# Kernel tuning notes

Hardware: AMD Instinct MI355X
Metric: run time of the kernel (lower is better)

Reference implementation:

```python
import jax, jax.numpy as jnp
import numpy as np

EPS = 1e-6
N_HEADS = 16
D_NOPE = 128   # qk_nope_head_dim == head_dim
D_ROPE = 64    # qk_rope_head_dim == head_dim // 2


def rmsnorm(x, g):
    # matches torch RMSNorm: normalize in fp32 then scale
    xf = x.astype(jnp.float32)
    n = xf * jax.lax.rsqrt(jnp.mean(xf * xf, axis=-1, keepdims=True) + EPS)
    return n.astype(x.dtype) * g


def rope(x):
    # x: [..., S, D]; rotary-embedding-torch convention: interleaved pairs, theta=10000
    S, D = x.shape[-2], x.shape[-1]
    freqs = 1.0 / (10000.0 ** (jnp.arange(0, D, 2, dtype=jnp.float32) / D))  # [D/2]
    ang = jnp.arange(S, dtype=jnp.float32)[:, None] * freqs                   # [S, D/2]
    ang = jnp.repeat(ang, 2, axis=-1)                                         # [S, D]
    cos, sin = jnp.cos(ang), jnp.sin(ang)
    x2 = x.reshape(*x.shape[:-1], D // 2, 2)
    xr = jnp.stack([-x2[..., 1], x2[..., 0]], axis=-1).reshape(x.shape)
    return x * cos + xr * sin


def setup_inputs() -> dict:
    key = jax.random.key(0)
    ks = jax.random.split(key, 9)
    def w(k, shape):
        return jax.random.normal(k, shape, dtype=jnp.float32) * (shape[0] ** -0.5)
    return {
        "x": jax.random.normal(ks[0], (2, 2048, 2048), dtype=jnp.float32),
        "w_dq": w(ks[1], (2048, 512)),
        "g_q": jnp.ones((512,), dtype=jnp.float32),
        "w_uq": w(ks[2], (512, 3072)),
        "w_dkv": w(ks[3], (2048, 512)),
        "g_kv": jnp.ones((512,), dtype=jnp.float32),
        "w_ukrope": w(ks[4], (2048, 64)),
        "w_uv": w(ks[5], (512, 2048)),
        "w_uknope": w(ks[6], (512, 2048)),
        "w_o": w(ks[7], (2048, 2048)),
    }


def reference(x, w_dq, g_q, w_uq, w_dkv, g_kv, w_ukrope, w_uv, w_uknope, w_o):
    B, S, _ = x.shape
    H, Dn, Dr = N_HEADS, D_NOPE, D_ROPE

    # low-rank KV path
    kv = rmsnorm(x @ w_dkv, g_kv)                                    # [B,S,512]
    k_nope = (kv @ w_uknope).reshape(B, S, H, Dn).transpose(0, 2, 1, 3)  # [B,H,S,Dn]
    v = (kv @ w_uv).reshape(B, S, H, Dn).transpose(0, 2, 1, 3)           # [B,H,S,Dn]
    k_rope = rope(x @ w_ukrope)                                      # [B,S,Dr] shared across heads

    # low-rank Q path
    q = rmsnorm(x @ w_dq, g_q) @ w_uq                                # [B,S,H*(Dn+Dr)]
    q = q.reshape(B, S, H, Dn + Dr).transpose(0, 2, 1, 3)            # [B,H,S,Dn+Dr]
    q_nope, q_rope = q[..., :Dn], rope(q[..., Dn:])

    # causal SDPA with head-shared rope keys folded into scores
    scale = 1.0 / jnp.sqrt(jnp.float32(Dn + Dr))
    scores = jnp.einsum("bhqd,bhkd->bhqk", q_nope, k_nope)
    scores = scores + jnp.einsum("bhqd,bkd->bhqk", q_rope, k_rope)
    scores = scores * scale
    causal = jnp.tril(jnp.ones((S, S), dtype=bool))
    scores = jnp.where(causal, scores, -jnp.inf)
    attn = jax.nn.softmax(scores, axis=-1)
    out = jnp.einsum("bhqk,bhkd->bhqd", attn, v)                     # [B,H,S,Dn]
    out = out.transpose(0, 2, 1, 3).reshape(B, S, H * Dn)
    return out @ w_o
```

## Files before the change

### kernel.cpp

```cpp
#include <hip/hip_runtime.h>
#include <hip/hip_bf16.h>


#define S_ 2048
#define H_ 16

typedef __bf16 bf16_t;
typedef __bf16 bf16x8 __attribute__((ext_vector_type(8)));
typedef __bf16 bf16x4_t __attribute__((ext_vector_type(4)));
typedef float f32x4 __attribute__((ext_vector_type(4)));

#define ASYNC_COPY16(gsrc, ldst)                                              \
  __builtin_amdgcn_global_load_lds(                                           \
      (const __attribute__((address_space(1))) void*)(gsrc),                  \
      (__attribute__((address_space(3))) void*)(ldst), 16, 0, 0)

#define QSCALE 0.1041177003f
#define FIXM 16.0f

struct TWDesc { const float* src; bf16_t* dst; int K, N, boff; };
struct TW7 { TWDesc d[7]; };

__global__ __launch_bounds__(256) void prep_all(const float* __restrict__ x,
                                                bf16_t* __restrict__ xb,
                                                float2* __restrict__ tab,
                                                TW7 t7) {
  __shared__ float t[32][33];
  int bid = blockIdx.x;
  int tid = threadIdx.x;
  if (bid < 8192) {
    int i = bid * 256 + tid;
    float4 v = ((const float4*)x)[i];
    bf16x4_t o = {(bf16_t)v.x, (bf16_t)v.y, (bf16_t)v.z, (bf16_t)v.w};
    ((bf16x4_t*)xb)[i] = o;
  } else if (bid < 8448) {
    int i = (bid - 8192) * 256 + tid;
    int j = i & 31, s = i >> 5;
    float freq = powf(10000.f, -(float)(2 * j) / 64.f);
    float ang = (float)s * freq;
    tab[i] = make_float2(cosf(ang), sinf(ang));
  } else {
    int e = 0;
#pragma unroll
    for (int i = 1; i < 7; i++)
      if (bid >= t7.d[i].boff) e = i;
    const float* src = t7.d[e].src;
    bf16_t* dst = t7.d[e].dst;
    int K = t7.d[e].K, N = t7.d[e].N;
    int lb = bid - t7.d[e].boff;
    int nx = N >> 5;
    int n0 = (lb % nx) * 32, k0 = (lb / nx) * 32;
    int tx = tid & 31, ty = tid >> 5;
#pragma unroll
    for (int i = 0; i < 4; i++)
      t[ty + i * 8][tx] = src[(size_t)(k0 + ty + i * 8) * N + n0 + tx];
    __syncthreads();
#pragma unroll
    for (int i = 0; i < 4; i++)
      dst[(size_t)(n0 + ty + i * 8) * K + k0 + tx] = (bf16_t)t[tx][ty + i * 8];
  }
}

template <typename OT, int MODE>
__global__ __launch_bounds__(256) void gemm_bt(const bf16_t* __restrict__ A,
                                               const bf16_t* __restrict__ Bt,
                                               OT* __restrict__ C, int M, int N,
                                               int K, int lda) {
  __shared__ bf16_t Asm[2][128 * 32];
  __shared__ bf16_t Bsm[2][128 * 32];
  int tid = threadIdx.x;
  int w = tid >> 6, lane = tid & 63;
  int lrow = lane & 15, lgrp = lane >> 4;
  int wr = w >> 1, wc = w & 1;
  int bm = blockIdx.y * 128, bn = blockIdx.x * 128;

  const bf16_t* Ab = A + (size_t)bm * lda;
  const bf16_t* Bb = Bt + (size_t)bn * K;

  int srow = (w << 5) + (lane >> 2);
  int schunk = lane & 3;

  int ra[4], rb[4];
#pragma unroll
  for (int m = 0; m < 4; m++) {
    int rowA = wr * 64 + m * 16 + lrow;
    ra[m] = rowA * 64 + ((lgrp * 16) ^ (((rowA >> 1) & 3) << 4));
    int rowB = wc * 64 + m * 16 + lrow;
    rb[m] = rowB * 64 + ((lgrp * 16) ^ (((rowB >> 1) & 3) << 4));
  }

  f32x4 acc[4][4] = {};

  auto stage = [&](int k0, int bufi) {
#pragma unroll
    for (int j = 0; j < 2; j++) {
      int row = srow + j * 16;
      int cs = schunk ^ ((row >> 1) & 3);
      ASYNC_COPY16(Ab + (size_t)row * lda + k0 + cs * 8,
                   (char*)Asm[bufi] + (w << 11) + (j << 10));
      ASYNC_COPY16(Bb + (size_t)row * K + k0 + cs * 8,
                   (char*)Bsm[bufi] + (w << 11) + (j << 10));
    }
  };

  const int niter = K >> 5;
  stage(0, 0);
  __syncthreads();
  int cur = 0;
#pragma unroll 1
  for (int kt = 0; kt < niter; kt++) {
    if (kt + 1 < niter) stage((kt + 1) << 5, cur ^ 1);
    bf16x8 af[4], bfr[4];
#pragma unroll
    for (int m = 0; m < 4; m++) {
      af[m] = *(const bf16x8*)((const char*)Asm[cur] + ra[m]);
      bfr[m] = *(const bf16x8*)((const char*)Bsm[cur] + rb[m]);
    }
#pragma unroll
    for (int m = 0; m < 4; m++)
#pragma unroll
      for (int n = 0; n < 4; n++)
        acc[m][n] =
            __builtin_amdgcn_mfma_f32_16x16x32_bf16(af[m], bfr[n], acc[m][n], 0, 0, 0);
    __syncthreads();
    cur ^= 1;
  }

#pragma unroll
  for (int m = 0; m < 4; m++)
#pragma unroll
    for (int n = 0; n < 4; n++)
#pragma unroll
      for (int j = 0; j < 4; j++) {
        int row = bm + wr * 64 + m * 16 + lgrp * 4 + j;
        int col = bn + wc * 64 + n * 16 + lrow;
        float val = acc[m][n][j];
        if (MODE == 0) {
          C[(size_t)row * N + col] = (OT)val;
        } else if (MODE == 6) {
          if (col < 1024) {
            ((bf16_t*)C)[(size_t)row * 1024 + col] = (bf16_t)val;
          } else if (col < 1088) {
            float* krf = (float*)((bf16_t*)C + (size_t)M * 1024);
            krf[(size_t)row * 64 + (col - 1024)] = val;
          }
        }
      }
}

__global__ __launch_bounds__(512) void gemm_qkv(const bf16_t* __restrict__ y,
                                                const bf16_t* __restrict__ uq_t,
                                                const bf16_t* __restrict__ ukn_t,
                                                bf16_t* __restrict__ Qp,
                                                bf16_t* __restrict__ Kp) {
  const int K = 512, lda = 1024;
  __shared__ bf16_t Asm[2][256 * 32];
  __shared__ bf16_t Bsm[2][128 * 32];
  int tid = threadIdx.x;
  int w = tid >> 6, lane = tid & 63;
  int lrow = lane & 15, lgrp = lane >> 4;
  int wr = w >> 1, wc = w & 1;
  int bnx = blockIdx.x;
  bool qpath = bnx < 24;
  const bf16_t* A = qpath ? y : (y + 512);
  const bf16_t* Bt = qpath ? uq_t : ukn_t;
  int bm = blockIdx.y * 256;
  int bn = (qpath ? bnx : bnx - 24) * 128;

  const bf16_t* Ab = A + (size_t)bm * lda;
  const bf16_t* Bb = Bt + (size_t)bn * K;

  int arow0 = tid >> 2, apos = tid & 3;
  int arow1 = arow0 + 128;

  int ra[4], rb[4];
#pragma unroll
  for (int m = 0; m < 4; m++) {
    int rowA = wr * 64 + m * 16 + lrow;
    ra[m] = rowA * 64 + ((lgrp * 16) ^ (((rowA >> 1) & 3) << 4));
    int rowB = wc * 64 + m * 16 + lrow;
    rb[m] = rowB * 64 + ((lgrp * 16) ^ (((rowB >> 1) & 3) << 4));
  }

  f32x4 acc[4][4] = {};

  auto stage = [&](int k0, int bufi) {
    int cs0 = apos ^ ((arow0 >> 1) & 3);
    ASYNC_COPY16(Ab + (size_t)arow0 * lda + k0 + cs0 * 8,
                 (char*)Asm[bufi] + tid * 16);
    int cs1 = apos ^ ((arow1 >> 1) & 3);
    ASYNC_COPY16(Ab + (size_t)arow1 * lda + k0 + cs1 * 8,
                 (char*)Asm[bufi] + (tid + 512) * 16);
    int cs2 = apos ^ ((arow0 >> 1) & 3);
    ASYNC_COPY16(Bb + (size_t)arow0 * K + k0 + cs2 * 8,
                 (char*)Bsm[bufi] + tid * 16);
  };

  const int niter = K >> 5;
  stage(0, 0);
  __syncthreads();
  int cur = 0;
#pragma unroll 1
  for (int kt = 0; kt < niter; kt++) {
    if (kt + 1 < niter) stage((kt + 1) << 5, cur ^ 1);
    bf16x8 af[4], bfr[4];
#pragma unroll
    for (int m = 0; m < 4; m++) {
      af[m] = *(const bf16x8*)((const char*)Asm[cur] + ra[m]);
      bfr[m] = *(const bf16x8*)((const char*)Bsm[cur] + rb[m]);
    }
#pragma unroll
    for (int m = 0; m < 4; m++)
#pragma unroll
      for (int n = 0; n < 4; n++)
        acc[m][n] =
            __builtin_amdgcn_mfma_f32_16x16x32_bf16(af[m], bfr[n], acc[m][n], 0, 0, 0);
    __syncthreads();
    cur ^= 1;
  }

#pragma unroll
  for (int m = 0; m < 4; m++)
#pragma unroll
    for (int n = 0; n < 4; n++) {
      int col = bn + wc * 64 + n * 16 + lrow;
      int row0 = bm + wr * 64 + m * 16 + lgrp * 4;
      if (!qpath && col >= 2048) {
        int c2 = col - 2048;
        int h = c2 >> 7, d = c2 & 127;
        bf16_t* VtP = Kp + (size_t)32 * S_ * 192;
        int b = row0 >> 11, s0 = row0 & (S_ - 1);
        bf16x4_t v4 = {(bf16_t)acc[m][n][0], (bf16_t)acc[m][n][1],
                       (bf16_t)acc[m][n][2], (bf16_t)acc[m][n][3]};
        *(bf16x4_t*)(VtP + ((size_t)((b << 4) + h) * 128 + d) * S_ + s0) = v4;
      } else {
#pragma unroll
        for (int j = 0; j < 4; j++) {
          int row = row0 + j;
          float val = acc[m][n][j];
          int b = row >> 11, s = row & (S_ - 1);
          if (qpath) {
            unsigned h = (unsigned)col / 192u, f = (unsigned)col % 192u;
            Qp[((size_t)((b << 4) + h) * S_ + s) * 192 + f] =
                (bf16_t)(val * QSCALE);
          } else {
            int h = col >> 7, d = col & 127;
            Kp[((size_t)((b << 4) + h) * S_ + s) * 192 + d] = (bf16_t)val;
          }
        }
      }
    }
}

__global__ __launch_bounds__(256) void rmsnorm_both(bf16_t* __restrict__ y,
                                                    const float* __restrict__ g_q,
                                                    const float* __restrict__ g_kv) {
  int bid = blockIdx.x;
  int row = bid >> 1, seg = bid & 1;
  const float* g = seg ? g_kv : g_q;
  bf16_t* p = y + (size_t)row * 1024 + seg * 512;
  int t = threadIdx.x;
  float v0 = (float)p[t], v1 = (float)p[t + 256];
  __shared__ float red[256];
  red[t] = v0 * v0 + v1 * v1;
  __syncthreads();
  for (int s = 128; s > 0; s >>= 1) {
    if (t < s) red[t] += red[t + s];
    __syncthreads();
  }
  float r = rsqrtf(red[0] / 512.f + 1e-6f);
  p[t] = (bf16_t)(v0 * r * g[t]);
  p[t + 256] = (bf16_t)(v1 * r * g[t + 256]);
}

__global__ __launch_bounds__(256) void rope_both(const float* __restrict__ krf,
                                                 const float2* __restrict__ tab,
                                                 bf16_t* __restrict__ Kp,
                                                 bf16_t* __restrict__ Qp) {
  int i = blockIdx.x * 256 + threadIdx.x;
  if (i < 4096 * 32) {
    int j = i & 31, row = i >> 5;
    int b = row >> 11, s = row & (S_ - 1);
    float v0 = krf[(size_t)row * 64 + 2 * j];
    float v1 = krf[(size_t)row * 64 + 2 * j + 1];
    float2 cs = tab[(s << 5) + j];
    bf16_t r0 = (bf16_t)(v0 * cs.x - v1 * cs.y);
    bf16_t r1 = (bf16_t)(v1 * cs.x + v0 * cs.y);
    union { bf16_t h[2]; unsigned u; } pk;
    pk.h[0] = r0; pk.h[1] = r1;
#pragma unroll
    for (int h = 0; h < 16; h++) {
      size_t base = ((size_t)((b << 4) + h) * S_ + s) * 192 + 128 + 2 * j;
      *(unsigned*)(Kp + base) = pk.u;
    }
  } else {
    int i2 = i - 4096 * 32;
    int j = i2 & 31;
    int s = (i2 >> 5) & (S_ - 1);
    int bh = i2 >> 16;
    float2 cs = tab[(s << 5) + j];
    size_t base = ((size_t)bh * S_ + s) * 192 + 128 + 2 * j;
    float x0 = (float)Qp[base], x1 = (float)Qp[base + 1];
    Qp[base] = (bf16_t)(x0 * cs.x - x1 * cs.y);
    Qp[base + 1] = (bf16_t)(x1 * cs.x + x0 * cs.y);
  }
}

__global__ __launch_bounds__(512) void flash_attn5(
    const bf16_t* __restrict__ Qp,
    const bf16_t* __restrict__ Kp,
    const bf16_t* __restrict__ Vt,
    bf16_t* __restrict__ o) {
  __shared__ alignas(16) char kls[2 * 64 * 384];
  __shared__ alignas(16) char vls[2 * 128 * 128];
  __shared__ alignas(16) bf16_t psh[8][16 * 64];

  int bid = blockIdx.x;
  int rest = bid >> 3;
  int p = rest & 7;
  int bh = (bid & 7) + ((rest >> 3) << 3);
  int b = bh >> 4;

  int tid = threadIdx.x;
  int w = tid >> 6;
  int lane = tid & 63;
  int lrow = lane & 15;
  int lgrp = lane >> 4;
  bf16_t* pw = &psh[w][0];

  const char* Kbh = (const char*)(Kp + (size_t)bh * S_ * 192);
  const char* Vbh = (const char*)(Vt + (size_t)bh * 128 * S_);

  int ksrc[3], vsrc[2];
#pragma unroll
  for (int r = 0; r < 3; r++) {
    int c = tid + r * 512;
    int row = c / 24, pos = c - row * 24;
    ksrc[r] = row * 384 + ((pos ^ (row & 7)) << 4);
  }
#pragma unroll
  for (int r = 0; r < 2; r++) {
    int c = tid + r * 512;
    int d = c >> 3, pos = c & 7;
    vsrc[r] = d * 4096 + ((pos ^ (d & 7)) << 4);
  }

  int kchk[6], vchk[2];
#pragma unroll
  for (int ks = 0; ks < 6; ks++)
    kchk[ks] = (((lgrp + ks * 4) ^ (lrow & 7)) << 4) + lrow * 384;
#pragma unroll
  for (int ks = 0; ks < 2; ks++)
    vchk[ks] = (((lgrp + ks * 4) ^ (lrow & 7)) << 4) + lrow * 128;

#pragma unroll 1
  for (int half = 0; half < 2; half++) {
    const int qt = half ? p : (15 - p);
    const int qb = qt * 128 + w * 16;
    const bf16_t* Qb = Qp + ((size_t)bh * S_ + qb) * 192;

    bf16x8 qf[6];
#pragma unroll
    for (int ks = 0; ks < 6; ks++)
      qf[ks] = *(const bf16x8*)(Qb + (size_t)lrow * 192 + ks * 32 + lgrp * 8);

    f32x4 acc[8];
#pragma unroll
    for (int i = 0; i < 8; i++) acc[i] = f32x4{0.f, 0.f, 0.f, 0.f};
    float lsum[4] = {0.f, 0.f, 0.f, 0.f};

    const int nk = 2 * qt + 2;
    {
      const char* kb = Kbh;
#pragma unroll
      for (int r = 0; r < 3; r++)
        ASYNC_COPY16(kb + ksrc[r], kls + (tid + r * 512) * 16);
#pragma unroll
      for (int r = 0; r < 2; r++)
        ASYNC_COPY16(Vbh + vsrc[r], vls + (tid + r * 512) * 16);
    }
    __syncthreads();

    int cur = 0;
#pragma unroll 1
    for (int kt = 0; kt < nk; kt++) {
      if (kt + 1 < nk) {
        const char* kb = Kbh + (size_t)(kt + 1) * (64 * 384);
        char* kd = kls + (cur ^ 1) * 24576;
#pragma unroll
        for (int r = 0; r < 3; r++)
          ASYNC_COPY16(kb + ksrc[r], kd + (tid + r * 512) * 16);
        const char* vb2 = Vbh + (size_t)(kt + 1) * 128;
        char* vd = vls + (cur ^ 1) * 16384;
#pragma unroll
        for (int r = 0; r < 2; r++)
          ASYNC_COPY16(vb2 + vsrc[r], vd + (tid + r * 512) * 16);
      }

      const char* kbuf = kls + cur * 24576;
      f32x4 sc[4];
#pragma unroll
      for (int cb = 0; cb < 4; cb++) {
        f32x4 s = f32x4{0.f, 0.f, 0.f, 0.f};
        const char* kp = kbuf + cb * 6144;
#pragma unroll
        for (int ks = 0; ks < 6; ks++) {
          bf16x8 kf = *(const bf16x8*)(kp + kchk[ks]);
          s = __builtin_amdgcn_mfma_f32_16x16x32_bf16(qf[ks], kf, s, 0, 0, 0);
        }
        sc[cb] = s;
      }
      if (kt >= 2 * qt) {
#pragma unroll
        for (int cb = 0; cb < 4; cb++)
#pragma unroll
          for (int r = 0; r < 4; r++) {
            int col = kt * 64 + cb * 16 + lrow;
            int row = qb + lgrp * 4 + r;
            if (col > row) sc[cb][r] = -1e30f;
          }
      }
#pragma unroll
      for (int r = 0; r < 4; r++) {
        float ps = 0.f;
#pragma unroll
        for (int cb = 0; cb < 4; cb++) {
          float e = exp2f(sc[cb][r] - FIXM);
          sc[cb][r] = e;
          ps += e;
        }
        lsum[r] += ps;
      }
#pragma unroll
      for (int r = 0; r < 4; r++) {
        int row = lgrp * 4 + r;
#pragma unroll
        for (int cb = 0; cb < 4; cb++) {
          int byte = (row * 128 + (cb * 16 + lrow) * 2) ^ ((row & 7) << 4);
          *(bf16_t*)((char*)pw + byte) = (bf16_t)sc[cb][r];
        }
      }
      bf16x8 pa[2];
#pragma unroll
      for (int ks = 0; ks < 2; ks++) {
        int byte = (lrow * 128 + ks * 64 + lgrp * 16) ^ ((lrow & 7) << 4);
        pa[ks] = *(const bf16x8*)((char*)pw + byte);
      }
      const char* vbuf = vls + cur * 16384;
#pragma unroll
      for (int cbv = 0; cbv < 8; cbv++) {
        const char* vp = vbuf + cbv * 2048;
        f32x4 a = acc[cbv];
#pragma unroll
        for (int ks = 0; ks < 2; ks++) {
          bf16x8 vf = *(const bf16x8*)(vp + vchk[ks]);
          a = __builtin_amdgcn_mfma_f32_16x16x32_bf16(pa[ks], vf, a, 0, 0, 0);
        }
        acc[cbv] = a;
      }
      __syncthreads();
      cur ^= 1;
    }
#pragma unroll
    for (int r = 0; r < 4; r++) {
      float s = lsum[r];
      s += __shfl_xor(s, 1);
      s += __shfl_xor(s, 2);
      s += __shfl_xor(s, 4);
      s += __shfl_xor(s, 8);
      float inv = 1.f / s;
      int row = qb + lgrp * 4 + r;
      bf16_t* op = o + (size_t)(b * S_ + row) * 2048 + (bh & 15) * 128;
#pragma unroll
      for (int cbv = 0; cbv < 8; cbv++)
        op[cbv * 16 + lrow] = (bf16_t)(acc[cbv][r] * inv);
    }
  }
}

extern "C" void kernel_launch(void* const* d_in, const int* in_sizes, int n_in,
                              void* d_out, int out_size, void* d_ws, size_t ws_size,
                              hipStream_t stream) {
  const float* x        = (const float*)d_in[0];
  const float* w_dq     = (const float*)d_in[1];
  const float* g_q      = (const float*)d_in[2];
  const float* w_uq     = (const float*)d_in[3];
  const float* w_dkv    = (const float*)d_in[4];
  const float* g_kv     = (const float*)d_in[5];
  const float* w_ukrope = (const float*)d_in[6];
  const float* w_uv     = (const float*)d_in[7];
  const float* w_uknope = (const float*)d_in[8];
  const float* w_o      = (const float*)d_in[9];
  float* out = (float*)d_out;

  const int M = 4096;
  bf16_t* wb = (bf16_t*)d_ws;
  size_t off = 0;
  bf16_t* xb   = wb + off; off += (size_t)M * 2048;
  bf16_t* y    = wb + off; off += (size_t)M * 1024;
  float*  krf  = (float*)(wb + off); off += (size_t)M * 128;
  bf16_t* dq_t = wb + off; off += (size_t)512 * 2048;
  bf16_t* dkv_t= wb + off; off += (size_t)512 * 2048;
  bf16_t* ukr_t= wb + off; off += (size_t)128 * 2048;
  bf16_t* uq_t = wb + off; off += (size_t)3072 * 512;
  bf16_t* ukn_t= wb + off; off += (size_t)2048 * 512;
  bf16_t* uv_t = wb + off; off += (size_t)2048 * 512;
  bf16_t* o_t  = wb + off; off += (size_t)2048 * 2048;
  bf16_t* Qp   = wb + off; off += (size_t)32 * S_ * 192;
  bf16_t* Kp   = wb + off; off += (size_t)32 * S_ * 192;
  bf16_t* Vt   = wb + off; off += (size_t)32 * 128 * S_;
  float2* tab  = (float2*)(wb + off); off += (size_t)S_ * 32 * 4;
  bf16_t* ao = xb;
  (void)dkv_t; (void)ukr_t; (void)uv_t;

  dim3 blk(256);
  TW7 t7;
  t7.d[0] = {w_dq,     dq_t,  2048, 512,  8448};
  t7.d[1] = {w_dkv,    dkv_t, 2048, 512,  9472};
  t7.d[2] = {w_ukrope, ukr_t, 2048, 64,   10496};
  t7.d[3] = {w_uq,     uq_t,  512,  3072, 10624};
  t7.d[4] = {w_uknope, ukn_t, 512,  2048, 12160};
  t7.d[5] = {w_uv,     uv_t,  512,  2048, 13184};
  t7.d[6] = {w_o,      o_t,   2048, 2048, 14208};
  prep_all<<<18304, blk, 0, stream>>>(x, xb, tab, t7);
  gemm_bt<bf16_t, 6><<<dim3(9, 32), blk, 0, stream>>>(xb, dq_t, y, M, 1152, 2048,
                                                      2048);
  rmsnorm_both<<<8192, blk, 0, stream>>>(y, g_q, g_kv);
  gemm_qkv<<<dim3(56, 16), dim3(512), 0, stream>>>(y, uq_t, ukn_t, Qp, Kp);
  rope_both<<<8704, blk, 0, stream>>>(krf, tab, Kp, Qp);
  flash_attn5<<<256, dim3(512), 0, stream>>>(Qp, Kp, Vt, ao);
  gemm_bt<float, 0><<<dim3(16, 32), blk, 0, stream>>>(ao, o_t, out, M, 2048, 2048,
                                                      2048);
}
```

Before: 251.2 us.

## Use larger 256x128 tile GEMM for output projection and raise MFMA priority

Replaces the output projection GEMM with a new 512-thread kernel using 256x128 tiles, double-buffered async LDS copies and swizzled LDS layout, launched on a 16x16 grid. This is meant to improve operand reuse and cut the number of workgroups, at the cost of fewer blocks to spread across CUs. The flash attention loop also wraps its MFMA sections in s_setprio to favour matrix instructions over other waves' work.

```diff
diff --git a/kernel.cpp b/kernel.cpp
--- a/kernel.cpp
+++ b/kernel.cpp
@@ -148,6 +148,82 @@
       }
 }
 
+__global__ __launch_bounds__(512) void gemm_bt2(const bf16_t* __restrict__ A,
+                                                const bf16_t* __restrict__ Bt,
+                                                float* __restrict__ C, int M,
+                                                int N, int K, int lda) {
+  __shared__ bf16_t Asm[2][256 * 32];
+  __shared__ bf16_t Bsm[2][128 * 32];
+  int tid = threadIdx.x;
+  int w = tid >> 6, lane = tid & 63;
+  int lrow = lane & 15, lgrp = lane >> 4;
+  int wr = w >> 1, wc = w & 1;
+  int bm = blockIdx.y * 256, bn = blockIdx.x * 128;
+
+  const bf16_t* Ab = A + (size_t)bm * lda;
+  const bf16_t* Bb = Bt + (size_t)bn * K;
+
+  int arow0 = tid >> 2, apos = tid & 3;
+  int arow1 = arow0 + 128;
+
+  int ra[4], rb[4];
+#pragma unroll
+  for (int m = 0; m < 4; m++) {
+    int rowA = wr * 64 + m * 16 + lrow;
+    ra[m] = rowA * 64 + ((lgrp * 16) ^ (((rowA >> 1) & 3) << 4));
+    int rowB = wc * 64 + m * 16 + lrow;
+    rb[m] = rowB * 64 + ((lgrp * 16) ^ (((rowB >> 1) & 3) << 4));
+  }
+
+  f32x4 acc[4][4] = {};
+
+  auto stage = [&](int k0, int bufi) {
+    int cs0 = apos ^ ((arow0 >> 1) & 3);
+    ASYNC_COPY16(Ab + (size_t)arow0 * lda + k0 + cs0 * 8,
+                 (char*)Asm[bufi] + tid * 16);
+    int cs1 = apos ^ ((arow1 >> 1) & 3);
+    ASYNC_COPY16(Ab + (size_t)arow1 * lda + k0 + cs1 * 8,
+                 (char*)Asm[bufi] + (tid + 512) * 16);
+    int cs2 = apos ^ ((arow0 >> 1) & 3);
+    ASYNC_COPY16(Bb + (size_t)arow0 * K + k0 + cs2 * 8,
+                 (char*)Bsm[bufi] + tid * 16);
+  };
+
+  const int niter = K >> 5;
+  stage(0, 0);
+  __syncthreads();
+  int cur = 0;
+#pragma unroll 1
+  for (int kt = 0; kt < niter; kt++) {
+    if (kt + 1 < niter) stage((kt + 1) << 5, cur ^ 1);
+    bf16x8 af[4], bfr[4];
+#pragma unroll
+    for (int m = 0; m < 4; m++) {
+      af[m] = *(const bf16x8*)((const char*)Asm[cur] + ra[m]);
+      bfr[m] = *(const bf16x8*)((const char*)Bsm[cur] + rb[m]);
+    }
+#pragma unroll
+    for (int m = 0; m < 4; m++)
+#pragma unroll
+      for (int n = 0; n < 4; n++)
+        acc[m][n] =
+            __builtin_amdgcn_mfma_f32_16x16x32_bf16(af[m], bfr[n], acc[m][n], 0, 0, 0);
+    __syncthreads();
+    cur ^= 1;
+  }
+
+#pragma unroll
+  for (int m = 0; m < 4; m++)
+#pragma unroll
+    for (int n = 0; n < 4; n++)
+#pragma unroll
+      for (int j = 0; j < 4; j++) {
+        int row = bm + wr * 64 + m * 16 + lgrp * 4 + j;
+        int col = bn + wc * 64 + n * 16 + lrow;
+        C[(size_t)row * N + col] = acc[m][n][j];
+      }
+}
+
 __global__ __launch_bounds__(512) void gemm_qkv(const bf16_t* __restrict__ y,
                                                 const bf16_t* __restrict__ uq_t,
                                                 const bf16_t* __restrict__ ukn_t,
@@ -399,6 +475,7 @@
 
       const char* kbuf = kls + cur * 24576;
       f32x4 sc[4];
+      __builtin_amdgcn_s_setprio(1);
 #pragma unroll
       for (int cb = 0; cb < 4; cb++) {
         f32x4 s = f32x4{0.f, 0.f, 0.f, 0.f};
@@ -410,6 +487,7 @@
         }
         sc[cb] = s;
       }
+      __builtin_amdgcn_s_setprio(0);
       if (kt >= 2 * qt) {
 #pragma unroll
         for (int cb = 0; cb < 4; cb++)
@@ -447,6 +525,7 @@
         pa[ks] = *(const bf16x8*)((char*)pw + byte);
       }
       const char* vbuf = vls + cur * 16384;
+      __builtin_amdgcn_s_setprio(1);
 #pragma unroll
       for (int cbv = 0; cbv < 8; cbv++) {
         const char* vp = vbuf + cbv * 2048;
@@ -458,6 +537,7 @@
         }
         acc[cbv] = a;
       }
+      __builtin_amdgcn_s_setprio(0);
       __syncthreads();
       cur ^= 1;
     }
@@ -529,6 +609,6 @@
   gemm_qkv<<<dim3(56, 16), dim3(512), 0, stream>>>(y, uq_t, ukn_t, Qp, Kp);
   rope_both<<<8704, blk, 0, stream>>>(krf, tab, Kp, Qp);
   flash_attn5<<<256, dim3(512), 0, stream>>>(Qp, Kp, Vt, ao);
-  gemm_bt<float, 0><<<dim3(16, 32), blk, 0, stream>>>(ao, o_t, out, M, 2048, 2048,
-                                                      2048);
-}
+  gemm_bt2<<<dim3(16, 16), dim3(512), 0, stream>>>(ao, o_t, out, M, 2048, 2048,
+                                                   2048);
+}
```

Result: slower. 260.3 us (+3.6%).
